# Kernel optimization log

Measured on AMD Instinct MI355X. Metric: run time of the kernel, lower is better.

The kernel has to match this reference:

```python
import jax, jax.numpy as jnp
import numpy as np

N, E = 50000, 800000
IN_DIM, HID, OUT, HEADS = 128, 128, 64, 4
C1 = HID // HEADS  # 32 per-head channels in gat1
NEG_SLOPE = 0.2


def _gat_conv(x, src, dst, W, a_src, a_dst, b, heads, ch):
    """PyG GATConv (inference): gather -> edge attention -> segment softmax -> scatter."""
    n = x.shape[0]
    h = (x @ W).reshape(n, heads, ch)                      # [N,H,C]
    alpha_src = jnp.einsum('nhc,hc->nh', h, a_src)         # [N,H]
    alpha_dst = jnp.einsum('nhc,hc->nh', h, a_dst)         # [N,H]
    e = jax.nn.leaky_relu(alpha_src[src] + alpha_dst[dst], NEG_SLOPE)  # [E,H]
    m = jax.ops.segment_max(e, dst, num_segments=n)        # per-target max (stable softmax)
    e = jnp.exp(e - m[dst])
    denom = jax.ops.segment_sum(e, dst, num_segments=n)
    alpha = e / (denom[dst] + 1e-16)                       # [E,H]
    out = jax.ops.segment_sum(h[src] * alpha[:, :, None], dst, num_segments=n)  # [N,H,C]
    return out.reshape(n, heads * ch) + b


def setup_inputs() -> dict:
    key = jax.random.key(0)
    ks = jax.random.split(key, 16)
    x = jax.random.normal(ks[0], (N, IN_DIM), dtype=jnp.float32)
    edge_index = jax.random.randint(ks[1], (2, E), 0, N, dtype=jnp.int64)
    s = lambda fan_in: 1.0 / np.sqrt(fan_in)
    return {
        'x': x,
        'edge_index': edge_index,
        'W1': jax.random.normal(ks[2], (IN_DIM, HEADS * C1), jnp.float32) * s(IN_DIM),
        'a_src1': jax.random.normal(ks[3], (HEADS, C1), jnp.float32) * s(C1),
        'a_dst1': jax.random.normal(ks[4], (HEADS, C1), jnp.float32) * s(C1),
        'b1': jnp.zeros((HID,), jnp.float32),
        'W2': jax.random.normal(ks[5], (HID, OUT), jnp.float32) * s(HID),
        'a_src2': jax.random.normal(ks[6], (1, OUT), jnp.float32) * s(OUT),
        'a_dst2': jax.random.normal(ks[7], (1, OUT), jnp.float32) * s(OUT),
        'b2': jnp.zeros((OUT,), jnp.float32),
        'pw1': jax.random.normal(ks[8], (OUT, OUT), jnp.float32) * s(OUT),
        'pb1': jnp.zeros((OUT,), jnp.float32),
        'pw2': jax.random.normal(ks[9], (OUT, OUT), jnp.float32) * s(OUT),
        'pb2': jnp.zeros((OUT,), jnp.float32),
    }


def reference(x, edge_index, W1, a_src1, a_dst1, b1, W2, a_src2, a_dst2, b2, pw1, pb1, pw2, pb2):
    n = x.shape[0]
    # PyG GATConv add_self_loops=True
    loops = jnp.arange(n, dtype=edge_index.dtype)
    src = jnp.concatenate([edge_index[0], loops])
    dst = jnp.concatenate([edge_index[1], loops])
    h = jax.nn.elu(_gat_conv(x, src, dst, W1, a_src1, a_dst1, b1, HEADS, C1))
    h = jax.nn.elu(_gat_conv(h, src, dst, W2, a_src2, a_dst2, b2, 1, OUT))
    # origin_proj: Linear -> ReLU -> Linear
    h = jax.nn.relu(h @ pw1 + pb1)
    return h @ pw2 + pb2
```

## Files before the change

kernel.cpp:

```cpp
#include <hip/hip_runtime.h>
#include <math.h>

#define N_NODES 50000
#define N_EDGES 800000
#define ET (N_EDGES + N_NODES)
#define IN_DIM 128
#define HID 128
#define OUT_DIM 64
#define BW 64
#define NBUCK ((N_NODES + BW - 1) / BW)
#define NBLK 832
#define EPB 1024
#define NT64 ((N_NODES + 63) / 64)

typedef __attribute__((ext_vector_type(8))) short bf16x8;
typedef __attribute__((ext_vector_type(4))) float f32x4;

__device__ __forceinline__ float lrelu(float x){ return x >= 0.f ? x : 0.2f * x; }
__device__ __forceinline__ float eluf(float x){ return x > 0.f ? x : expm1f(x); }
__device__ __forceinline__ unsigned f2bf(float f){
    unsigned u = __float_as_uint(f);
    return (u + 0x7fffu + ((u >> 16) & 1u)) >> 16;
}
__device__ __forceinline__ float bflo(unsigned u){ return __uint_as_float(u << 16); }
__device__ __forceinline__ float bfhi(unsigned u){ return __uint_as_float(u & 0xffff0000u); }

__global__ __launch_bounds__(256) void k_count_prep(
    const int* __restrict__ dst, int* __restrict__ C,
    const float* __restrict__ W1, const float* __restrict__ W2,
    unsigned* __restrict__ w1bT, unsigned* __restrict__ w2bT)
{
    __shared__ int cnt[NBUCK];
    const int tid = threadIdx.x, blk = blockIdx.x;
    if (blk == NBLK) {
        for (int idx = tid; idx < 8192; idx += 256) {
            const int n = idx & 127, kp = idx >> 7;
            w1bT[n * 64 + kp] = f2bf(W1[(2 * kp) * 128 + n])
                              | (f2bf(W1[(2 * kp + 1) * 128 + n]) << 16);
        }
        for (int idx = tid; idx < 4096; idx += 256) {
            const int n = idx & 63, kp = idx >> 6;
            w2bT[n * 64 + kp] = f2bf(W2[(2 * kp) * 64 + n])
                              | (f2bf(W2[(2 * kp + 1) * 64 + n]) << 16);
        }
        return;
    }
    for (int i = tid; i < NBUCK; i += 256) cnt[i] = 0;
    __syncthreads();
    #pragma unroll
    for (int j = 0; j < EPB / 256; j++) {
        const int e = blk * EPB + j * 256 + tid;
        if (e < ET) {
            const int d = (e < N_EDGES) ? dst[e] : (e - N_EDGES);
            atomicAdd(&cnt[d >> 6], 1);
        }
    }
    __syncthreads();
    for (int b = tid; b < NBUCK; b += 256) C[b * NBLK + blk] = cnt[b];
}

__global__ __launch_bounds__(256) void k_bsumA(const int* __restrict__ C, int* __restrict__ bsum2)
{
    __shared__ int red[4];
    int v = 0;
    for (int j = threadIdx.x; j < NBLK; j += 256) v += C[blockIdx.x * NBLK + j];
    #pragma unroll
    for (int off = 32; off > 0; off >>= 1) v += __shfl_down(v, off);
    if ((threadIdx.x & 63) == 0) red[threadIdx.x >> 6] = v;
    __syncthreads();
    if (threadIdx.x == 0) bsum2[blockIdx.x] = red[0] + red[1] + red[2] + red[3];
}

__global__ __launch_bounds__(1024) void k_bscanB(const int* __restrict__ bsum2, int* __restrict__ boff2)
{
    __shared__ int part[1024];
    const int t = threadIdx.x;
    int v = (t < NBUCK) ? bsum2[t] : 0;
    part[t] = v;
    __syncthreads();
    #pragma unroll
    for (int d = 1; d < 1024; d <<= 1) {
        int add = (t >= d) ? part[t - d] : 0;
        __syncthreads();
        part[t] += add;
        __syncthreads();
    }
    if (t < NBUCK) boff2[t] = part[t] - v;
    if (t == 0) boff2[NBUCK] = ET;
}

__global__ __launch_bounds__(1024) void k_cscanC(const int* __restrict__ C,
                                                 const int* __restrict__ boff2,
                                                 int* __restrict__ Cs)
{
    __shared__ int part[1024];
    const int t = threadIdx.x, b = blockIdx.x;
    int v = (t < NBLK) ? C[b * NBLK + t] : 0;
    part[t] = v;
    __syncthreads();
    #pragma unroll
    for (int d = 1; d < 1024; d <<= 1) {
        int add = (t >= d) ? part[t - d] : 0;
        __syncthreads();
        part[t] += add;
        __syncthreads();
    }
    if (t < NBLK) Cs[b * NBLK + t] = boff2[b] + part[t] - v;
}

__global__ __launch_bounds__(256, 2) void k_gemm1(
    const float* __restrict__ x, const unsigned* __restrict__ w1bT,
    const float* __restrict__ a_s, const float* __restrict__ a_d,
    unsigned* __restrict__ h1b, float* __restrict__ as1, float* __restrict__ ad1)
{
    __shared__ unsigned sWt[128 * 68];
    __shared__ unsigned sxb[64 * 68];
    const int tid = threadIdx.x;
    const int wave = tid >> 6;
    const int lane = tid & 63;
    const int ll   = lane & 15;
    const int quad = lane >> 4;
    const int n0 = blockIdx.x * 64;

    for (int idx = tid; idx < 2048; idx += 256) {
        const uint4 w = ((const uint4*)w1bT)[idx];
        const int n = idx >> 4, q = idx & 15;
        unsigned* dp = &sWt[n * 68 + 4 * q];
        dp[0] = w.x; dp[1] = w.y; dp[2] = w.z; dp[3] = w.w;
    }
    for (int idx = tid; idx < 4096; idx += 256) {
        const int node = idx >> 6, kp = idx & 63;
        const int n = n0 + node;
        unsigned pk = 0;
        if (n < N_NODES) {
            const float x0 = x[n * 128 + 2 * kp];
            const float x1 = x[n * 128 + 2 * kp + 1];
            pk = f2bf(x0) | (f2bf(x1) << 16);
        }
        sxb[node * 68 + kp] = pk;
    }
    __syncthreads();

    f32x4 acc[8];
    #pragma unroll
    for (int t = 0; t < 8; t++) acc[t] = (f32x4){0.f, 0.f, 0.f, 0.f};

    #pragma unroll
    for (int kk = 0; kk < 4; kk++) {
        const int kpo = 16 * kk + 4 * quad;
        const bf16x8 a = *(const bf16x8*)&sxb[(16 * wave + ll) * 68 + kpo];
        #pragma unroll
        for (int t = 0; t < 8; t++) {
            const bf16x8 b = *(const bf16x8*)&sWt[(16 * t + ll) * 68 + kpo];
            acc[t] = __builtin_amdgcn_mfma_f32_16x16x32_bf16(a, b, acc[t], 0, 0, 0);
        }
    }

    float as_v[8], ad_v[8];
    #pragma unroll
    for (int t = 0; t < 8; t++) { as_v[t] = a_s[16 * t + ll]; ad_v[t] = a_d[16 * t + ll]; }
    unsigned short* h1u = (unsigned short*)h1b;
    #pragma unroll
    for (int r = 0; r < 4; r++) {
        const int n = n0 + 16 * wave + 4 * quad + r;
        float ps0 = acc[0][r] * as_v[0] + acc[1][r] * as_v[1];
        float ps1 = acc[2][r] * as_v[2] + acc[3][r] * as_v[3];
        float ps2 = acc[4][r] * as_v[4] + acc[5][r] * as_v[5];
        float ps3 = acc[6][r] * as_v[6] + acc[7][r] * as_v[7];
        float pd0 = acc[0][r] * ad_v[0] + acc[1][r] * ad_v[1];
        float pd1 = acc[2][r] * ad_v[2] + acc[3][r] * ad_v[3];
        float pd2 = acc[4][r] * ad_v[4] + acc[5][r] * ad_v[5];
        float pd3 = acc[6][r] * ad_v[6] + acc[7][r] * ad_v[7];
        #pragma unroll
        for (int off = 1; off < 16; off <<= 1) {
            ps0 += __shfl_xor(ps0, off); ps1 += __shfl_xor(ps1, off);
            ps2 += __shfl_xor(ps2, off); ps3 += __shfl_xor(ps3, off);
            pd0 += __shfl_xor(pd0, off); pd1 += __shfl_xor(pd1, off);
            pd2 += __shfl_xor(pd2, off); pd3 += __shfl_xor(pd3, off);
        }
        if (n < N_NODES) {
            #pragma unroll
            for (int t = 0; t < 8; t++)
                h1u[n * 128 + 16 * t + ll] = (unsigned short)f2bf(acc[t][r]);
            if (ll == 0) {
                as1[n * 4 + 0] = ps0; as1[n * 4 + 1] = ps1;
                as1[n * 4 + 2] = ps2; as1[n * 4 + 3] = ps3;
                ad1[n * 4 + 0] = pd0; ad1[n * 4 + 1] = pd1;
                ad1[n * 4 + 2] = pd2; ad1[n * 4 + 3] = pd3;
            }
        }
    }
}

__global__ __launch_bounds__(256) void k_part2(
    const int* __restrict__ src, const int* __restrict__ dst,
    const int* __restrict__ Cs, uint2* __restrict__ part)
{
    __shared__ int base[NBUCK];
    __shared__ int cnt[NBUCK];
    const int tid = threadIdx.x, blk = blockIdx.x;
    for (int b = tid; b < NBUCK; b += 256) { base[b] = Cs[b * NBLK + blk]; cnt[b] = 0; }
    __syncthreads();
    #pragma unroll
    for (int j = 0; j < EPB / 256; j++) {
        const int e = blk * EPB + j * 256 + tid;
        if (e < ET) {
            int s, d;
            if (e < N_EDGES) { s = src[e]; d = dst[e]; } else { s = d = e - N_EDGES; }
            const int b = d >> 6;
            const int r = atomicAdd(&cnt[b], 1);
            part[base[b] + r] = make_uint2((unsigned)d, (unsigned)s);
        }
    }
}

__global__ __launch_bounds__(256) void k_scat2(const int* __restrict__ boff2,
                                               const uint2* __restrict__ part,
                                               const float* __restrict__ as1,
                                               const float* __restrict__ ad1,
                                               int* __restrict__ rowptr,
                                               int* __restrict__ csr_src,
                                               float4* __restrict__ w1e)
{
    __shared__ int cnt64[BW];
    __shared__ int nbase[BW];
    __shared__ float4 sad[BW];
    const int b = blockIdx.x, tid = threadIdx.x;
    const int n0 = b * BW;
    const int lo = boff2[b], hi = boff2[b + 1];
    if (tid < BW) {
        cnt64[tid] = 0;
        const int n = n0 + tid;
        sad[tid] = (n < N_NODES) ? ((const float4*)ad1)[n] : make_float4(0.f, 0.f, 0.f, 0.f);
    }
    __syncthreads();
    for (int i = lo + tid; i < hi; i += 256) {
        atomicAdd(&cnt64[part[i].x & (BW - 1)], 1);
    }
    __syncthreads();
    if (tid < BW) {
        int v = cnt64[tid];
        int incl = v;
        #pragma unroll
        for (int off = 1; off < 64; off <<= 1) {
            int t2 = __shfl_up(incl, off);
            if (tid >= off) incl += t2;
        }
        const int excl = incl - v;
        nbase[tid] = excl;
        const int n = n0 + tid;
        if (n < N_NODES) rowptr[n] = lo + excl;
        cnt64[tid] = 0;
    }
    if (b == 0 && tid == 0) rowptr[N_NODES] = ET;
    __syncthreads();
    for (int i = lo + tid; i < hi; i += 256) {
        const uint2 p = part[i];
        const int dn = (int)p.x & (BW - 1);
        const int s  = (int)p.y;
        const int r = atomicAdd(&cnt64[dn], 1);
        const int pos = lo + nbase[dn] + r;
        csr_src[pos] = s;
        const float4 av = ((const float4*)as1)[s];
        const float4 dv = sad[dn];
        float4 w;
        w.x = expf(lrelu(av.x + dv.x));
        w.y = expf(lrelu(av.y + dv.y));
        w.z = expf(lrelu(av.z + dv.z));
        w.w = expf(lrelu(av.w + dv.w));
        w1e[pos] = w;
    }
}

__global__ __launch_bounds__(256) void k_aggr1(
    const int* __restrict__ rowptr, const int* __restrict__ csr_src,
    const float* __restrict__ w1e,
    const uint4* __restrict__ h1u4, const float* __restrict__ b1,
    unsigned* __restrict__ hEb)
{
    const int d  = blockIdx.x * 16 + (threadIdx.x >> 4);
    const int c8 = threadIdx.x & 15;
    const int hd = c8 >> 2;
    const int r0 = rowptr[d], r1 = rowptr[d + 1];
    float den = 0.f;
    float acc[8];
    #pragma unroll
    for (int m = 0; m < 8; m++) acc[m] = 0.f;
    int i = r0;
    for (; i + 4 <= r1; i += 4) {
        const int s0 = csr_src[i],     s1 = csr_src[i + 1];
        const int s2 = csr_src[i + 2], s3 = csr_src[i + 3];
        const float w0 = w1e[(i    ) * 4 + hd];
        const float w1 = w1e[(i + 1) * 4 + hd];
        const float w2 = w1e[(i + 2) * 4 + hd];
        const float w3 = w1e[(i + 3) * 4 + hd];
        const uint4 u0 = h1u4[s0 * 16 + c8];
        const uint4 u1 = h1u4[s1 * 16 + c8];
        const uint4 u2 = h1u4[s2 * 16 + c8];
        const uint4 u3 = h1u4[s3 * 16 + c8];
        den += (w0 + w1) + (w2 + w3);
        acc[0] = fmaf(bflo(u0.x), w0, acc[0]); acc[1] = fmaf(bfhi(u0.x), w0, acc[1]);
        acc[2] = fmaf(bflo(u0.y), w0, acc[2]); acc[3] = fmaf(bfhi(u0.y), w0, acc[3]);
        acc[4] = fmaf(bflo(u0.z), w0, acc[4]); acc[5] = fmaf(bfhi(u0.z), w0, acc[5]);
        acc[6] = fmaf(bflo(u0.w), w0, acc[6]); acc[7] = fmaf(bfhi(u0.w), w0, acc[7]);
        acc[0] = fmaf(bflo(u1.x), w1, acc[0]); acc[1] = fmaf(bfhi(u1.x), w1, acc[1]);
        acc[2] = fmaf(bflo(u1.y), w1, acc[2]); acc[3] = fmaf(bfhi(u1.y), w1, acc[3]);
        acc[4] = fmaf(bflo(u1.z), w1, acc[4]); acc[5] = fmaf(bfhi(u1.z), w1, acc[5]);
        acc[6] = fmaf(bflo(u1.w), w1, acc[6]); acc[7] = fmaf(bfhi(u1.w), w1, acc[7]);
        acc[0] = fmaf(bflo(u2.x), w2, acc[0]); acc[1] = fmaf(bfhi(u2.x), w2, acc[1]);
        acc[2] = fmaf(bflo(u2.y), w2, acc[2]); acc[3] = fmaf(bfhi(u2.y), w2, acc[3]);
        acc[4] = fmaf(bflo(u2.z), w2, acc[4]); acc[5] = fmaf(bfhi(u2.z), w2, acc[5]);
        acc[6] = fmaf(bflo(u2.w), w2, acc[6]); acc[7] = fmaf(bfhi(u2.w), w2, acc[7]);
        acc[0] = fmaf(bflo(u3.x), w3, acc[0]); acc[1] = fmaf(bfhi(u3.x), w3, acc[1]);
        acc[2] = fmaf(bflo(u3.y), w3, acc[2]); acc[3] = fmaf(bfhi(u3.y), w3, acc[3]);
        acc[4] = fmaf(bflo(u3.z), w3, acc[4]); acc[5] = fmaf(bfhi(u3.z), w3, acc[5]);
        acc[6] = fmaf(bflo(u3.w), w3, acc[6]); acc[7] = fmaf(bfhi(u3.w), w3, acc[7]);
    }
    for (; i < r1; ++i) {
        const int s = csr_src[i];
        const float w = w1e[i * 4 + hd];
        const uint4 u = h1u4[s * 16 + c8];
        den += w;
        acc[0] = fmaf(bflo(u.x), w, acc[0]); acc[1] = fmaf(bfhi(u.x), w, acc[1]);
        acc[2] = fmaf(bflo(u.y), w, acc[2]); acc[3] = fmaf(bfhi(u.y), w, acc[3]);
        acc[4] = fmaf(bflo(u.z), w, acc[4]); acc[5] = fmaf(bfhi(u.z), w, acc[5]);
        acc[6] = fmaf(bflo(u.w), w, acc[6]); acc[7] = fmaf(bfhi(u.w), w, acc[7]);
    }
    const float inv = 1.f / (den + 1e-16f);
    const float4 bA = ((const float4*)b1)[2 * c8];
    const float4 bB = ((const float4*)b1)[2 * c8 + 1];
    const float v0 = eluf(acc[0] * inv + bA.x);
    const float v1 = eluf(acc[1] * inv + bA.y);
    const float v2 = eluf(acc[2] * inv + bA.z);
    const float v3 = eluf(acc[3] * inv + bA.w);
    const float v4 = eluf(acc[4] * inv + bB.x);
    const float v5 = eluf(acc[5] * inv + bB.y);
    const float v6 = eluf(acc[6] * inv + bB.z);
    const float v7 = eluf(acc[7] * inv + bB.w);
    uint4 o;
    o.x = f2bf(v0) | (f2bf(v1) << 16);
    o.y = f2bf(v2) | (f2bf(v3) << 16);
    o.z = f2bf(v4) | (f2bf(v5) << 16);
    o.w = f2bf(v6) | (f2bf(v7) << 16);
    ((uint4*)hEb)[d * 16 + c8] = o;
}

__global__ __launch_bounds__(256, 4) void k_layer2(
    const unsigned* __restrict__ hEb, const unsigned* __restrict__ w2bT,
    const float* __restrict__ a_s2, const float* __restrict__ a_d2,
    unsigned* __restrict__ h2b, float* __restrict__ as2, float* __restrict__ ad2)
{
    __shared__ unsigned sWt[64 * 68];
    __shared__ unsigned sxb[64 * 68];
    const int tid = threadIdx.x;
    const int wave = tid >> 6;
    const int lane = tid & 63;
    const int ll   = lane & 15;
    const int quad = lane >> 4;
    const int n0 = blockIdx.x * 64;

    for (int idx = tid; idx < 1024; idx += 256) {
        const uint4 w = ((const uint4*)w2bT)[idx];
        const int n = idx >> 4, q = idx & 15;
        unsigned* dp = &sWt[n * 68 + 4 * q];
        dp[0] = w.x; dp[1] = w.y; dp[2] = w.z; dp[3] = w.w;
    }
    const uint4* hE4 = (const uint4*)hEb;
    for (int idx = tid; idx < 1024; idx += 256) {
        const int node = idx >> 4, q = idx & 15;
        const int n = n0 + node;
        uint4 pk = make_uint4(0, 0, 0, 0);
        if (n < N_NODES) pk = hE4[n * 16 + q];
        unsigned* dstp = &sxb[node * 68 + 4 * q];
        dstp[0] = pk.x; dstp[1] = pk.y; dstp[2] = pk.z; dstp[3] = pk.w;
    }
    __syncthreads();

    f32x4 acc[4];
    #pragma unroll
    for (int t = 0; t < 4; t++) acc[t] = (f32x4){0.f, 0.f, 0.f, 0.f};

    #pragma unroll
    for (int kk = 0; kk < 4; kk++) {
        const int kpo = 16 * kk + 4 * quad;
        const bf16x8 a = *(const bf16x8*)&sxb[(16 * wave + ll) * 68 + kpo];
        #pragma unroll
        for (int t = 0; t < 4; t++) {
            const bf16x8 b = *(const bf16x8*)&sWt[(16 * t + ll) * 68 + kpo];
            acc[t] = __builtin_amdgcn_mfma_f32_16x16x32_bf16(a, b, acc[t], 0, 0, 0);
        }
    }

    float as_v[4], ad_v[4];
    #pragma unroll
    for (int t = 0; t < 4; t++) { as_v[t] = a_s2[16 * t + ll]; ad_v[t] = a_d2[16 * t + ll]; }
    unsigned short* h2u = (unsigned short*)h2b;
    #pragma unroll
    for (int r = 0; r < 4; r++) {
        const int n = n0 + 16 * wave + 4 * quad + r;
        float ps = acc[0][r] * as_v[0] + acc[1][r] * as_v[1]
                 + acc[2][r] * as_v[2] + acc[3][r] * as_v[3];
        float pd = acc[0][r] * ad_v[0] + acc[1][r] * ad_v[1]
                 + acc[2][r] * ad_v[2] + acc[3][r] * ad_v[3];
        #pragma unroll
        for (int off = 1; off < 16; off <<= 1) {
            ps += __shfl_xor(ps, off);
            pd += __shfl_xor(pd, off);
        }
        if (n < N_NODES) {
            #pragma unroll
            for (int t = 0; t < 4; t++)
                h2u[n * 64 + 16 * t + ll] = (unsigned short)f2bf(acc[t][r]);
            if (ll == 0) { as2[n] = ps; ad2[n] = pd; }
        }
    }
}

__global__ __launch_bounds__(512, 4) void k_tail(
    const int* __restrict__ rowptr, const int* __restrict__ csr_src,
    const float* __restrict__ as2, const float* __restrict__ ad2,
    const uint4* __restrict__ h2u4, const float* __restrict__ b2,
    const float* __restrict__ pw1, const float* __restrict__ pb1,
    const float* __restrict__ pw2, const float* __restrict__ pb2,
    float* __restrict__ out)
{
    __shared__ float s1[64 * 64];
    __shared__ float s2[64 * 64];
    __shared__ float so[64][68];
    __shared__ float sp[64][68];
    const int tid = threadIdx.x;
    const int n0 = blockIdx.x * 64;

    for (int i = tid; i < 1024; i += 512) {
        ((float4*)s1)[i] = ((const float4*)pw1)[i];
        ((float4*)s2)[i] = ((const float4*)pw2)[i];
    }

    {
        const int dl = tid >> 3;
        const int c8 = tid & 7;
        const int d = n0 + dl;
        float acc[8];
        #pragma unroll
        for (int m = 0; m < 8; m++) acc[m] = 0.f;
        float v0 = 0.f, v1 = 0.f, v2 = 0.f, v3 = 0.f;
        float v4 = 0.f, v5 = 0.f, v6 = 0.f, v7 = 0.f;
        if (d < N_NODES) {
            const int r0 = rowptr[d], r1 = rowptr[d + 1];
            const float adv = ad2[d];
            float den = 0.f;
            int i = r0;
            for (; i + 4 <= r1; i += 4) {
                const int s0 = csr_src[i],      s1_ = csr_src[i + 1];
                const int s2_ = csr_src[i + 2], s3_ = csr_src[i + 3];
                const float e0 = as2[s0], e1 = as2[s1_], e2 = as2[s2_], e3 = as2[s3_];
                const uint4 u0 = h2u4[s0  * 8 + c8];
                const uint4 u1 = h2u4[s1_ * 8 + c8];
                const uint4 u2 = h2u4[s2_ * 8 + c8];
                const uint4 u3 = h2u4[s3_ * 8 + c8];
                const float w0 = expf(lrelu(e0 + adv));
                const float w1 = expf(lrelu(e1 + adv));
                const float w2 = expf(lrelu(e2 + adv));
                const float w3 = expf(lrelu(e3 + adv));
                den += (w0 + w1) + (w2 + w3);
                acc[0] = fmaf(bflo(u0.x), w0, acc[0]); acc[1] = fmaf(bfhi(u0.x), w0, acc[1]);
                acc[2] = fmaf(bflo(u0.y), w0, acc[2]); acc[3] = fmaf(bfhi(u0.y), w0, acc[3]);
                acc[4] = fmaf(bflo(u0.z), w0, acc[4]); acc[5] = fmaf(bfhi(u0.z), w0, acc[5]);
                acc[6] = fmaf(bflo(u0.w), w0, acc[6]); acc[7] = fmaf(bfhi(u0.w), w0, acc[7]);
                acc[0] = fmaf(bflo(u1.x), w1, acc[0]); acc[1] = fmaf(bfhi(u1.x), w1, acc[1]);
                acc[2] = fmaf(bflo(u1.y), w1, acc[2]); acc[3] = fmaf(bfhi(u1.y), w1, acc[3]);
                acc[4] = fmaf(bflo(u1.z), w1, acc[4]); acc[5] = fmaf(bfhi(u1.z), w1, acc[5]);
                acc[6] = fmaf(bflo(u1.w), w1, acc[6]); acc[7] = fmaf(bfhi(u1.w), w1, acc[7]);
                acc[0] = fmaf(bflo(u2.x), w2, acc[0]); acc[1] = fmaf(bfhi(u2.x), w2, acc[1]);
                acc[2] = fmaf(bflo(u2.y), w2, acc[2]); acc[3] = fmaf(bfhi(u2.y), w2, acc[3]);
                acc[4] = fmaf(bflo(u2.z), w2, acc[4]); acc[5] = fmaf(bfhi(u2.z), w2, acc[5]);
                acc[6] = fmaf(bflo(u2.w), w2, acc[6]); acc[7] = fmaf(bfhi(u2.w), w2, acc[7]);
                acc[0] = fmaf(bflo(u3.x), w3, acc[0]); acc[1] = fmaf(bfhi(u3.x), w3, acc[1]);
                acc[2] = fmaf(bflo(u3.y), w3, acc[2]); acc[3] = fmaf(bfhi(u3.y), w3, acc[3]);
                acc[4] = fmaf(bflo(u3.z), w3, acc[4]); acc[5] = fmaf(bfhi(u3.z), w3, acc[5]);
                acc[6] = fmaf(bflo(u3.w), w3, acc[6]); acc[7] = fmaf(bfhi(u3.w), w3, acc[7]);
            }
            for (; i < r1; ++i) {
                const int s = csr_src[i];
                const float w = expf(lrelu(as2[s] + adv));
                const uint4 u = h2u4[s * 8 + c8];
                den += w;
                acc[0] = fmaf(bflo(u.x), w, acc[0]); acc[1] = fmaf(bfhi(u.x), w, acc[1]);
                acc[2] = fmaf(bflo(u.y), w, acc[2]); acc[3] = fmaf(bfhi(u.y), w, acc[3]);
                acc[4] = fmaf(bflo(u.z), w, acc[4]); acc[5] = fmaf(bfhi(u.z), w, acc[5]);
                acc[6] = fmaf(bflo(u.w), w, acc[6]); acc[7] = fmaf(bfhi(u.w), w, acc[7]);
            }
            const float inv = 1.f / (den + 1e-16f);
            const float4 bA = ((const float4*)b2)[2 * c8];
            const float4 bB = ((const float4*)b2)[2 * c8 + 1];
            v0 = eluf(acc[0] * inv + bA.x);
            v1 = eluf(acc[1] * inv + bA.y);
            v2 = eluf(acc[2] * inv + bA.z);
            v3 = eluf(acc[3] * inv + bA.w);
            v4 = eluf(acc[4] * inv + bB.x);
            v5 = eluf(acc[5] * inv + bB.y);
            v6 = eluf(acc[6] * inv + bB.z);
            v7 = eluf(acc[7] * inv + bB.w);
        }
        *(float4*)&so[dl][8 * c8]     = make_float4(v0, v1, v2, v3);
        *(float4*)&so[dl][8 * c8 + 4] = make_float4(v4, v5, v6, v7);
    }
    __syncthreads();

    const int cg = tid & 15;
    const int ng = tid >> 4;
    const float4 pb1_4 = ((const float4*)pb1)[cg];
    const float4 pb2_4 = ((const float4*)pb2)[cg];
    float4 p[2];
    #pragma unroll
    for (int m = 0; m < 2; m++) p[m] = pb1_4;
    #pragma unroll 8
    for (int k = 0; k < 64; k++) {
        const float4 w = *(const float4*)&s1[k * 64 + 4 * cg];
        #pragma unroll
        for (int m = 0; m < 2; m++) {
            const float xv = so[2 * ng + m][k];
            p[m].x = fmaf(xv, w.x, p[m].x);
            p[m].y = fmaf(xv, w.y, p[m].y);
            p[m].z = fmaf(xv, w.z, p[m].z);
            p[m].w = fmaf(xv, w.w, p[m].w);
        }
    }
    #pragma unroll
    for (int m = 0; m < 2; m++) {
        p[m].x = fmaxf(p[m].x, 0.f); p[m].y = fmaxf(p[m].y, 0.f);
        p[m].z = fmaxf(p[m].z, 0.f); p[m].w = fmaxf(p[m].w, 0.f);
        *(float4*)&sp[2 * ng + m][4 * cg] = p[m];
    }
    __syncthreads();

    float4 o[2];
    #pragma unroll
    for (int m = 0; m < 2; m++) o[m] = pb2_4;
    #pragma unroll 8
    for (int k = 0; k < 64; k++) {
        const float4 w = *(const float4*)&s2[k * 64 + 4 * cg];
        #pragma unroll
        for (int m = 0; m < 2; m++) {
            const float xv = sp[2 * ng + m][k];
            o[m].x = fmaf(xv, w.x, o[m].x);
            o[m].y = fmaf(xv, w.y, o[m].y);
            o[m].z = fmaf(xv, w.z, o[m].z);
            o[m].w = fmaf(xv, w.w, o[m].w);
        }
    }
    #pragma unroll
    for (int m = 0; m < 2; m++) {
        const int n = n0 + 2 * ng + m;
        if (n < N_NODES) ((float4*)out)[n * 16 + cg] = o[m];
    }
}

extern "C" void kernel_launch(void* const* d_in, const int* in_sizes, int n_in,
                              void* d_out, int out_size, void* d_ws, size_t ws_size,
                              hipStream_t stream)
{
    const float* x      = (const float*)d_in[0];
    const int*   ei     = (const int*)d_in[1];
    const int*   src    = ei;
    const int*   dst    = ei + N_EDGES;
    const float* W1     = (const float*)d_in[2];
    const float* a_src1 = (const float*)d_in[3];
    const float* a_dst1 = (const float*)d_in[4];
    const float* b1     = (const float*)d_in[5];
    const float* W2     = (const float*)d_in[6];
    const float* a_src2 = (const float*)d_in[7];
    const float* a_dst2 = (const float*)d_in[8];
    const float* b2     = (const float*)d_in[9];
    const float* pw1    = (const float*)d_in[10];
    const float* pb1    = (const float*)d_in[11];
    const float* pw2    = (const float*)d_in[12];
    const float* pb2    = (const float*)d_in[13];

    uint2*  part = (uint2*)d_ws;
    float4* w1e  = (float4*)(part + ET);
    int* ibase   = (int*)(w1e + ET);
    int* rowptr  = ibase;
    int* C       = rowptr + 50004;
    int* Cs      = C + 650624;
    int* bsum2   = Cs + 650624;
    int* boff2   = bsum2 + 784;
    int* csr_src = boff2 + 784;
    unsigned* h1b = (unsigned*)(csr_src + 850000);
    unsigned* h2b = h1b + 3200000;
    float* fws   = (float*)(h2b + 1600000);
    float* as1   = fws;
    float* ad1   = as1 + 200000;
    unsigned* hEb = (unsigned*)(ad1 + 200000);
    float* as2   = (float*)(hEb + 3200000);
    float* ad2   = as2 + 50000;
    unsigned* w1bT = (unsigned*)(ad2 + 50000);
    unsigned* w2bT = w1bT + 8192;

    k_count_prep<<<NBLK + 1, 256, 0, stream>>>(dst, C, W1, W2, w1bT, w2bT);
    k_bsumA<<<NBUCK, 256, 0, stream>>>(C, bsum2);
    k_bscanB<<<1, 1024, 0, stream>>>(bsum2, boff2);
    k_cscanC<<<NBUCK, 1024, 0, stream>>>(C, boff2, Cs);

    k_gemm1<<<NT64, 256, 0, stream>>>(x, w1bT, a_src1, a_dst1, h1b, as1, ad1);

    k_part2<<<NBLK, 256, 0, stream>>>(src, dst, Cs, part);

    k_scat2<<<NBUCK, 256, 0, stream>>>(boff2, part, as1, ad1,
                                       rowptr, csr_src, w1e);

    k_aggr1<<<N_NODES / 16, 256, 0, stream>>>(rowptr, csr_src, (const float*)w1e,
                                              (const uint4*)h1b, b1, hEb);

    k_layer2<<<NT64, 256, 0, stream>>>(hEb, w2bT, a_src2, a_dst2, h2b, as2, ad2);

    k_tail<<<NT64, 512, 0, stream>>>(rowptr, csr_src, as2, ad2,
                                     (const uint4*)h2b, b2,
                                     pw1, pb1, pw2, pb2, (float*)d_out);
}
```

Measured before the change: 265.2 us.

## Shrink partition block count and fuse edge partitioning with GEMM1 launch

The edge-bucketing pass now uses 256 partition blocks of 3328 edges instead of 832 blocks of 1024. This shrinks the per-block bucket count matrix and its scans, so k_bsumA and k_cscanC become single-pass 256-thread kernels. The partition scatter and the first-layer GEMM are merged into one launch whose blocks branch by index, letting the independent work overlap and saving one launch. In exchange, each partition block does more serial work with more shared-memory atomic contention, and the fused kernel's shared-memory footprint is sized for the GEMM path.

```diff
diff --git a/kernel.cpp b/kernel.cpp
--- a/kernel.cpp
+++ b/kernel.cpp
@@ -9,8 +9,8 @@
 #define OUT_DIM 64
 #define BW 64
 #define NBUCK ((N_NODES + BW - 1) / BW)
-#define NBLK 832
-#define EPB 1024
+#define NBLK 256
+#define EPB 3328
 #define NT64 ((N_NODES + 63) / 64)
 
 typedef __attribute__((ext_vector_type(8))) short bf16x8;
@@ -62,8 +62,7 @@
 __global__ __launch_bounds__(256) void k_bsumA(const int* __restrict__ C, int* __restrict__ bsum2)
 {
     __shared__ int red[4];
-    int v = 0;
-    for (int j = threadIdx.x; j < NBLK; j += 256) v += C[blockIdx.x * NBLK + j];
+    int v = C[blockIdx.x * NBLK + threadIdx.x];
     #pragma unroll
     for (int off = 32; off > 0; off >>= 1) v += __shfl_down(v, off);
     if ((threadIdx.x & 63) == 0) red[threadIdx.x >> 6] = v;
@@ -89,127 +88,128 @@
     if (t == 0) boff2[NBUCK] = ET;
 }
 
-__global__ __launch_bounds__(1024) void k_cscanC(const int* __restrict__ C,
-                                                 const int* __restrict__ boff2,
-                                                 int* __restrict__ Cs)
-{
-    __shared__ int part[1024];
+__global__ __launch_bounds__(256) void k_cscanC(const int* __restrict__ C,
+                                                const int* __restrict__ boff2,
+                                                int* __restrict__ Cs)
+{
+    __shared__ int part[256];
     const int t = threadIdx.x, b = blockIdx.x;
-    int v = (t < NBLK) ? C[b * NBLK + t] : 0;
+    int v = C[b * NBLK + t];
     part[t] = v;
     __syncthreads();
     #pragma unroll
-    for (int d = 1; d < 1024; d <<= 1) {
+    for (int d = 1; d < 256; d <<= 1) {
         int add = (t >= d) ? part[t - d] : 0;
         __syncthreads();
         part[t] += add;
         __syncthreads();
     }
-    if (t < NBLK) Cs[b * NBLK + t] = boff2[b] + part[t] - v;
-}
-
-__global__ __launch_bounds__(256, 2) void k_gemm1(
+    Cs[b * NBLK + t] = boff2[b] + part[t] - v;
+}
+
+__global__ __launch_bounds__(256, 2) void k_part2_gemm1(
     const float* __restrict__ x, const unsigned* __restrict__ w1bT,
     const float* __restrict__ a_s, const float* __restrict__ a_d,
-    unsigned* __restrict__ h1b, float* __restrict__ as1, float* __restrict__ ad1)
-{
-    __shared__ unsigned sWt[128 * 68];
-    __shared__ unsigned sxb[64 * 68];
-    const int tid = threadIdx.x;
-    const int wave = tid >> 6;
-    const int lane = tid & 63;
-    const int ll   = lane & 15;
-    const int quad = lane >> 4;
-    const int n0 = blockIdx.x * 64;
-
-    for (int idx = tid; idx < 2048; idx += 256) {
-        const uint4 w = ((const uint4*)w1bT)[idx];
-        const int n = idx >> 4, q = idx & 15;
-        unsigned* dp = &sWt[n * 68 + 4 * q];
-        dp[0] = w.x; dp[1] = w.y; dp[2] = w.z; dp[3] = w.w;
-    }
-    for (int idx = tid; idx < 4096; idx += 256) {
-        const int node = idx >> 6, kp = idx & 63;
-        const int n = n0 + node;
-        unsigned pk = 0;
-        if (n < N_NODES) {
-            const float x0 = x[n * 128 + 2 * kp];
-            const float x1 = x[n * 128 + 2 * kp + 1];
-            pk = f2bf(x0) | (f2bf(x1) << 16);
-        }
-        sxb[node * 68 + kp] = pk;
-    }
-    __syncthreads();
-
-    f32x4 acc[8];
-    #pragma unroll
-    for (int t = 0; t < 8; t++) acc[t] = (f32x4){0.f, 0.f, 0.f, 0.f};
-
-    #pragma unroll
-    for (int kk = 0; kk < 4; kk++) {
-        const int kpo = 16 * kk + 4 * quad;
-        const bf16x8 a = *(const bf16x8*)&sxb[(16 * wave + ll) * 68 + kpo];
-        #pragma unroll
-        for (int t = 0; t < 8; t++) {
-            const bf16x8 b = *(const bf16x8*)&sWt[(16 * t + ll) * 68 + kpo];
-            acc[t] = __builtin_amdgcn_mfma_f32_16x16x32_bf16(a, b, acc[t], 0, 0, 0);
-        }
-    }
-
-    float as_v[8], ad_v[8];
-    #pragma unroll
-    for (int t = 0; t < 8; t++) { as_v[t] = a_s[16 * t + ll]; ad_v[t] = a_d[16 * t + ll]; }
-    unsigned short* h1u = (unsigned short*)h1b;
-    #pragma unroll
-    for (int r = 0; r < 4; r++) {
-        const int n = n0 + 16 * wave + 4 * quad + r;
-        float ps0 = acc[0][r] * as_v[0] + acc[1][r] * as_v[1];
-        float ps1 = acc[2][r] * as_v[2] + acc[3][r] * as_v[3];
-        float ps2 = acc[4][r] * as_v[4] + acc[5][r] * as_v[5];
-        float ps3 = acc[6][r] * as_v[6] + acc[7][r] * as_v[7];
-        float pd0 = acc[0][r] * ad_v[0] + acc[1][r] * ad_v[1];
-        float pd1 = acc[2][r] * ad_v[2] + acc[3][r] * ad_v[3];
-        float pd2 = acc[4][r] * ad_v[4] + acc[5][r] * ad_v[5];
-        float pd3 = acc[6][r] * ad_v[6] + acc[7][r] * ad_v[7];
-        #pragma unroll
-        for (int off = 1; off < 16; off <<= 1) {
-            ps0 += __shfl_xor(ps0, off); ps1 += __shfl_xor(ps1, off);
-            ps2 += __shfl_xor(ps2, off); ps3 += __shfl_xor(ps3, off);
-            pd0 += __shfl_xor(pd0, off); pd1 += __shfl_xor(pd1, off);
-            pd2 += __shfl_xor(pd2, off); pd3 += __shfl_xor(pd3, off);
-        }
-        if (n < N_NODES) {
-            #pragma unroll
-            for (int t = 0; t < 8; t++)
-                h1u[n * 128 + 16 * t + ll] = (unsigned short)f2bf(acc[t][r]);
-            if (ll == 0) {
-                as1[n * 4 + 0] = ps0; as1[n * 4 + 1] = ps1;
-                as1[n * 4 + 2] = ps2; as1[n * 4 + 3] = ps3;
-                ad1[n * 4 + 0] = pd0; ad1[n * 4 + 1] = pd1;
-                ad1[n * 4 + 2] = pd2; ad1[n * 4 + 3] = pd3;
-            }
-        }
-    }
-}
-
-__global__ __launch_bounds__(256) void k_part2(
+    unsigned* __restrict__ h1b, float* __restrict__ as1, float* __restrict__ ad1,
     const int* __restrict__ src, const int* __restrict__ dst,
     const int* __restrict__ Cs, uint2* __restrict__ part)
 {
-    __shared__ int base[NBUCK];
-    __shared__ int cnt[NBUCK];
-    const int tid = threadIdx.x, blk = blockIdx.x;
-    for (int b = tid; b < NBUCK; b += 256) { base[b] = Cs[b * NBLK + blk]; cnt[b] = 0; }
-    __syncthreads();
-    #pragma unroll
-    for (int j = 0; j < EPB / 256; j++) {
-        const int e = blk * EPB + j * 256 + tid;
-        if (e < ET) {
-            int s, d;
-            if (e < N_EDGES) { s = src[e]; d = dst[e]; } else { s = d = e - N_EDGES; }
-            const int b = d >> 6;
-            const int r = atomicAdd(&cnt[b], 1);
-            part[base[b] + r] = make_uint2((unsigned)d, (unsigned)s);
+    __shared__ unsigned smem[128 * 68 + 64 * 68];
+    const int tid = threadIdx.x;
+
+    if (blockIdx.x < NBLK) {
+        const int blk = blockIdx.x;
+        int* base = (int*)smem;
+        int* cnt  = (int*)smem + NBUCK;
+        for (int b = tid; b < NBUCK; b += 256) { base[b] = Cs[b * NBLK + blk]; cnt[b] = 0; }
+        __syncthreads();
+        #pragma unroll
+        for (int j = 0; j < EPB / 256; j++) {
+            const int e = blk * EPB + j * 256 + tid;
+            if (e < ET) {
+                int s, d;
+                if (e < N_EDGES) { s = src[e]; d = dst[e]; } else { s = d = e - N_EDGES; }
+                const int b = d >> 6;
+                const int r = atomicAdd(&cnt[b], 1);
+                part[base[b] + r] = make_uint2((unsigned)d, (unsigned)s);
+            }
+        }
+    } else {
+        unsigned* sWt = smem;
+        unsigned* sxb = smem + 128 * 68;
+        const int wave = tid >> 6;
+        const int lane = tid & 63;
+        const int ll   = lane & 15;
+        const int quad = lane >> 4;
+        const int n0 = (blockIdx.x - NBLK) * 64;
+
+        for (int idx = tid; idx < 2048; idx += 256) {
+            const uint4 w = ((const uint4*)w1bT)[idx];
+            const int n = idx >> 4, q = idx & 15;
+            unsigned* dp = &sWt[n * 68 + 4 * q];
+            dp[0] = w.x; dp[1] = w.y; dp[2] = w.z; dp[3] = w.w;
+        }
+        for (int idx = tid; idx < 4096; idx += 256) {
+            const int node = idx >> 6, kp = idx & 63;
+            const int n = n0 + node;
+            unsigned pk = 0;
+            if (n < N_NODES) {
+                const float x0 = x[n * 128 + 2 * kp];
+                const float x1 = x[n * 128 + 2 * kp + 1];
+                pk = f2bf(x0) | (f2bf(x1) << 16);
+            }
+            sxb[node * 68 + kp] = pk;
+        }
+        __syncthreads();
+
+        f32x4 acc[8];
+        #pragma unroll
+        for (int t = 0; t < 8; t++) acc[t] = (f32x4){0.f, 0.f, 0.f, 0.f};
+
+        #pragma unroll
+        for (int kk = 0; kk < 4; kk++) {
+            const int kpo = 16 * kk + 4 * quad;
+            const bf16x8 a = *(const bf16x8*)&sxb[(16 * wave + ll) * 68 + kpo];
+            #pragma unroll
+            for (int t = 0; t < 8; t++) {
+                const bf16x8 b = *(const bf16x8*)&sWt[(16 * t + ll) * 68 + kpo];
+                acc[t] = __builtin_amdgcn_mfma_f32_16x16x32_bf16(a, b, acc[t], 0, 0, 0);
+            }
+        }
+
+        float as_v[8], ad_v[8];
+        #pragma unroll
+        for (int t = 0; t < 8; t++) { as_v[t] = a_s[16 * t + ll]; ad_v[t] = a_d[16 * t + ll]; }
+        unsigned short* h1u = (unsigned short*)h1b;
+        #pragma unroll
+        for (int r = 0; r < 4; r++) {
+            const int n = n0 + 16 * wave + 4 * quad + r;
+            float ps0 = acc[0][r] * as_v[0] + acc[1][r] * as_v[1];
+            float ps1 = acc[2][r] * as_v[2] + acc[3][r] * as_v[3];
+            float ps2 = acc[4][r] * as_v[4] + acc[5][r] * as_v[5];
+            float ps3 = acc[6][r] * as_v[6] + acc[7][r] * as_v[7];
+            float pd0 = acc[0][r] * ad_v[0] + acc[1][r] * ad_v[1];
+            float pd1 = acc[2][r] * ad_v[2] + acc[3][r] * ad_v[3];
+            float pd2 = acc[4][r] * ad_v[4] + acc[5][r] * ad_v[5];
+            float pd3 = acc[6][r] * ad_v[6] + acc[7][r] * ad_v[7];
+            #pragma unroll
+            for (int off = 1; off < 16; off <<= 1) {
+                ps0 += __shfl_xor(ps0, off); ps1 += __shfl_xor(ps1, off);
+                ps2 += __shfl_xor(ps2, off); ps3 += __shfl_xor(ps3, off);
+                pd0 += __shfl_xor(pd0, off); pd1 += __shfl_xor(pd1, off);
+                pd2 += __shfl_xor(pd2, off); pd3 += __shfl_xor(pd3, off);
+            }
+            if (n < N_NODES) {
+                #pragma unroll
+                for (int t = 0; t < 8; t++)
+                    h1u[n * 128 + 16 * t + ll] = (unsigned short)f2bf(acc[t][r]);
+                if (ll == 0) {
+                    as1[n * 4 + 0] = ps0; as1[n * 4 + 1] = ps1;
+                    as1[n * 4 + 2] = ps2; as1[n * 4 + 3] = ps3;
+                    ad1[n * 4 + 0] = pd0; ad1[n * 4 + 1] = pd1;
+                    ad1[n * 4 + 2] = pd2; ad1[n * 4 + 3] = pd3;
+                }
+            }
         }
     }
 }
@@ -582,8 +582,8 @@
     int* ibase   = (int*)(w1e + ET);
     int* rowptr  = ibase;
     int* C       = rowptr + 50004;
-    int* Cs      = C + 650624;
-    int* bsum2   = Cs + 650624;
+    int* Cs      = C + 200192;
+    int* bsum2   = Cs + 200192;
     int* boff2   = bsum2 + 784;
     int* csr_src = boff2 + 784;
     unsigned* h1b = (unsigned*)(csr_src + 850000);
@@ -600,11 +600,11 @@
     k_count_prep<<<NBLK + 1, 256, 0, stream>>>(dst, C, W1, W2, w1bT, w2bT);
     k_bsumA<<<NBUCK, 256, 0, stream>>>(C, bsum2);
     k_bscanB<<<1, 1024, 0, stream>>>(bsum2, boff2);
-    k_cscanC<<<NBUCK, 1024, 0, stream>>>(C, boff2, Cs);
-
-    k_gemm1<<<NT64, 256, 0, stream>>>(x, w1bT, a_src1, a_dst1, h1b, as1, ad1);
-
-    k_part2<<<NBLK, 256, 0, stream>>>(src, dst, Cs, part);
+    k_cscanC<<<NBUCK, 256, 0, stream>>>(C, boff2, Cs);
+
+    k_part2_gemm1<<<NBLK + NT64, 256, 0, stream>>>(x, w1bT, a_src1, a_dst1,
+                                                   h1b, as1, ad1,
+                                                   src, dst, Cs, part);
 
     k_scat2<<<NBUCK, 256, 0, stream>>>(boff2, part, as1, ad1,
                                        rowptr, csr_src, w1e);
```

Result: faster. 246.8 us (-6.9%).
